# Kernel tuning notes

Hardware: AMD Instinct MI355X
Metric: run time of the kernel (lower is better)

The kernel has to match this reference:

```python
import jax, jax.numpy as jnp
import numpy as np

DILATIONS = (1, 2, 4, 8, 16, 32)
T_ENC = 168   # encoder context length
T_PRED = 24   # predict_sequence_length
FILTERS = 64
FEAT = 15
HIDDEN = 128
B = 2048


def setup_inputs() -> dict:
    key = jax.random.key(0)
    ks = jax.random.split(key, 12)
    w = lambda k, s: jax.random.normal(k, s, jnp.float32) * 0.05
    return {
        "decoder_features": jax.random.normal(ks[0], (B, T_PRED, FEAT), jnp.float32),
        "decoder_init_input": jax.random.normal(ks[1], (B, 1), jnp.float32),
        "encoder_outputs": jax.random.normal(ks[2], (len(DILATIONS), B, T_ENC, FILTERS), jnp.float32),
        "W1": w(ks[3], (FEAT + 1, FILTERS)), "b1": jnp.zeros((FILTERS,), jnp.float32),
        "W2": w(ks[4], (FILTERS, 2 * FILTERS)), "b2": jnp.zeros((2 * FILTERS,), jnp.float32),
        "W3": w(ks[5], (FILTERS, 2 * FILTERS)),
        "W4": w(ks[6], (FILTERS, 2 * FILTERS)), "b4": jnp.zeros((2 * FILTERS,), jnp.float32),
        "W5": w(ks[7], (FILTERS * len(DILATIONS), HIDDEN)), "b5": jnp.zeros((HIDDEN,), jnp.float32),
        "W6": w(ks[8], (HIDDEN, 1)), "b6": jnp.zeros((1,), jnp.float32),
    }


def reference(decoder_features, decoder_init_input, encoder_outputs,
              W1, b1, W2, b2, W3, W4, b4, W5, b5, W6, b6):
    L, Bd, Te, F = encoder_outputs.shape
    # Preallocated growing state buffer (the torch/keras code does tf.concat each step)
    bufs0 = jnp.concatenate(
        [encoder_outputs, jnp.zeros((L, Bd, T_PRED, F), encoder_outputs.dtype)], axis=2)

    def step(bufs, t):
        # Note: the source never updates prev_output, so (eval mode) this_input
        # always uses decoder_init_input concatenated with step-t features.
        this_input = jnp.concatenate(
            [decoder_init_input, decoder_features[:, t]], axis=-1)  # [B, FEAT+1]
        x = jnp.tanh(this_input @ W1 + b1)  # [B, F]
        skips_all = []
        for l, d in enumerate(DILATIONS):
            # encoder_outputs[l][:, -d, :] of a buffer of current length T_ENC + t
            state = jax.lax.dynamic_index_in_dim(
                bufs[l], T_ENC + t - d, axis=1, keepdims=False)  # [B, F]
            dc = state @ W2 + b2 + x @ W3  # [B, 2F]
            f, g = jnp.split(dc, 2, axis=1)
            gated = jnp.tanh(f) * jax.nn.sigmoid(g)  # [B, F]
            out = gated @ W4 + b4  # [B, 2F]
            skips, res = jnp.split(out, 2, axis=1)
            x = x + res
            bufs = bufs.at[l, :, T_ENC + t, :].set(x)
            skips_all.append(skips)
        sk = jax.nn.relu(jnp.concatenate(skips_all, axis=1))  # [B, F*L]
        h = jax.nn.relu(sk @ W5 + b5)  # [B, HIDDEN]
        y = h @ W6 + b6  # [B, 1]
        return bufs, y

    _, ys = jax.lax.scan(step, bufs0, jnp.arange(T_PRED))
    return jnp.transpose(ys, (1, 0, 2))  # [B, T_PRED, 1]
```

## Files before the change

kernel.cpp:

```cpp
#include <hip/hip_runtime.h>
#include <hip/hip_bf16.h>
#include <cstddef>

#define NB 2048
#define TENC 168
#define TPRED 24

typedef _Float16 h8 __attribute__((ext_vector_type(8)));
typedef float f4v __attribute__((ext_vector_type(4)));

#define LBAR() asm volatile("s_waitcnt lgkmcnt(0)\ns_barrier" ::: "memory")

__device__ __forceinline__ float tanh_fast(float v) {
  v = fminf(v, 15.0f);
  const float ex = __expf(2.0f * v);
  return (ex - 1.0f) * __builtin_amdgcn_rcpf(ex + 1.0f);
}
__device__ __forceinline__ float sig_fast(float v) {
  return __builtin_amdgcn_rcpf(1.0f + __expf(-v));
}

#define MFMA16(a, b, c) __builtin_amdgcn_mfma_f32_16x16x32_f16((a), (b), (c), 0, 0, 0)

__global__ __launch_bounds__(512, 1) void dec_phase1(
    const float* __restrict__ feat,
    const float* __restrict__ dinit,
    const float* __restrict__ enc,
    const float* __restrict__ W1,
    const float* __restrict__ b1,
    const float* __restrict__ W2,
    const float* __restrict__ b2,
    const float* __restrict__ W3,
    const float* __restrict__ W4,
    const float* __restrict__ b4,
    _Float16* __restrict__ skbuf,
    int t_steps)
{
  __shared__ _Float16 ring[23][16][72];
  __shared__ _Float16 g16v[2][16][72];
  __shared__ _Float16 xf16[16][72];
  __shared__ float    xf32[64][20];
  __shared__ _Float16 W43h[64][136];

  const int tid = threadIdx.x;
  const int w   = tid >> 6;
  const int ln  = tid & 63;
  const int i   = ln & 15;
  const int q   = ln >> 4;
  const int q8  = q * 8;
  const int e0  = blockIdx.x * 16;

  float* W3s  = (float*)&ring[0][0][0];
  float* W4rs = W3s + 64 * 128;
  for (int idx = tid; idx < 2048; idx += 512)
    ((float4*)W3s)[idx] = ((const float4*)W3)[idx];
  for (int idx = tid; idx < 1024; idx += 512) {
    const int row = idx >> 4, seg = idx & 15;
    *(float4*)&W4rs[row * 64 + seg * 4] = *(const float4*)&W4[row * 128 + 64 + seg * 4];
  }
  __syncthreads();
  {
    const int c = tid & 127, k0 = (tid >> 7) << 4;
    float acc[16];
    #pragma unroll
    for (int r = 0; r < 16; ++r) acc[r] = 0.0f;
    for (int m = 0; m < 64; ++m) {
      const float w3v = W3s[m * 128 + c];
      #pragma unroll
      for (int r = 0; r < 16; ++r) acc[r] += W4rs[(k0 + r) * 64 + m] * w3v;
    }
    #pragma unroll
    for (int r = 0; r < 16; ++r) W43h[k0 + r][c] = (_Float16)acc[r];
  }
  __syncthreads();

  const int fs = w & 3;
  const int cf = 16 * fs + i;
  const int cg = 64 + cf;
  const int cs = 16 * (w - 4) + i;

  h8 BW2f[2], BW2g[2], BW3f[2], BW3g[2], B43f[2], B43g[2], B4s[2], B4r[2];
  float b2f = 0.f, b2g = 0.f, b4s_b = 0.f, b4r_b = 0.f;
  if (w < 4) {
    #pragma unroll
    for (int kk = 0; kk < 2; ++kk)
      #pragma unroll
      for (int j = 0; j < 8; ++j) {
        const int k = kk * 32 + q8 + j;
        BW2f[kk][j] = (_Float16)W2[k * 128 + cf];
        BW2g[kk][j] = (_Float16)W2[k * 128 + cg];
        BW3f[kk][j] = (_Float16)W3[k * 128 + cf];
        BW3g[kk][j] = (_Float16)W3[k * 128 + cg];
        B43f[kk][j] = W43h[k][cf];
        B43g[kk][j] = W43h[k][cg];
      }
    b2f = b2[cf]; b2g = b2[cg];
  } else {
    #pragma unroll
    for (int kk = 0; kk < 2; ++kk)
      #pragma unroll
      for (int j = 0; j < 8; ++j) {
        const int k = kk * 32 + q8 + j;
        B4s[kk][j] = (_Float16)W4[k * 128 + cs];
        B4r[kk][j] = (_Float16)W4[k * 128 + 64 + cs];
      }
    b4s_b = b4[cs]; b4r_b = b4[64 + cs];
  }
  float w1r[16];
  #pragma unroll
  for (int ii = 0; ii < 16; ++ii) w1r[ii] = W1[ii * 64 + ln];
  const float b1r  = b1[ln];
  const float ini0 = dinit[e0 + 2 * w];
  const float ini1 = dinit[e0 + 2 * w + 1];

  for (int idx = tid; idx < 1920; idx += 512) {
    const int c = idx & 7, el = (idx >> 3) & 15, s = idx >> 7;
    int l, j;
    if (s == 0)      { l = 0; j = 0; }
    else if (s < 3)  { l = 1; j = s - 1; }
    else if (s < 7)  { l = 2; j = s - 3; }
    else             { l = 3; j = s - 7; }
    const int d = 1 << l;
    const float* ep = enc + (((size_t)l * NB + e0 + el) * TENC + (TENC + j - d)) * 64 + c * 8;
    h8 hv;
    #pragma unroll
    for (int u = 0; u < 8; ++u) hv[u] = (_Float16)ep[u];
    *(h8*)&ring[s][el][c * 8] = hv;
  }

  #pragma unroll
  for (int s = 0; s < 2; ++s) {
    const int el = 2 * w + s;
    const float* fp = feat + (size_t)(e0 + el) * TPRED * 15;
    float u = b1r + (s ? ini1 : ini0) * w1r[0];
    #pragma unroll
    for (int ii = 0; ii < 15; ++ii) u += fp[ii] * w1r[ii + 1];
    const float xv = tanh_fast(u);
    xf16[el][ln] = (_Float16)xv;
    xf32[ln][el] = xv;
  }
  LBAR();

  f4v Zf = {0,0,0,0}, Zg = {0,0,0,0}, xreg = {0,0,0,0};

  for (int t = 0; t < t_steps; ++t) {
    const int tn = (t + 1 < t_steps) ? t + 1 : t;
    f4v pfa[2], pfb[2], pfc[2];
    float2 pfd[2]; float pfe[2];
    #pragma unroll
    for (int s = 0; s < 2; ++s) {
      const float* fp = feat + ((size_t)(e0 + 2 * w + s) * TPRED + tn) * 15;
      pfa[s] = *(const f4v*)(fp);
      pfb[s] = *(const f4v*)(fp + 4);
      pfc[s] = *(const f4v*)(fp + 8);
      pfd[s] = *(const float2*)(fp + 12);
      pfe[s] = fp[14];
    }

    h8 s0a[4], s1a[4], s4a0, s4a1;
    f4v p4[4], p5[4];
    if (w < 4) {
      const int t4 = (t < 16) ? t : 0;
      const float* e4 = enc + (((size_t)4 * NB + e0 + i) * TENC + (152 + t4)) * 64 + q8;
      const float* e5 = enc + (((size_t)5 * NB + e0 + i) * TENC + (136 + t )) * 64 + q8;
      p4[0] = *(const f4v*)(e4);      p4[1] = *(const f4v*)(e4 + 4);
      p4[2] = *(const f4v*)(e4 + 32); p4[3] = *(const f4v*)(e4 + 36);
      p5[0] = *(const f4v*)(e5);      p5[1] = *(const f4v*)(e5 + 4);
      p5[2] = *(const f4v*)(e5 + 32); p5[3] = *(const f4v*)(e5 + 36);

      #pragma unroll
      for (int l = 0; l < 4; ++l) {
        const int d = 1 << l;
        const int slot = (d - 1) + (t & (d - 1));
        s0a[l] = *(const h8*)&ring[slot][i][q8];
        s1a[l] = *(const h8*)&ring[slot][i][32 + q8];
      }
      {
        const int slot4 = 15 + (t & 7);
        s4a0 = *(const h8*)&ring[slot4][i][q8];
        s4a1 = *(const h8*)&ring[slot4][i][32 + q8];
      }

      const h8 a2 = *(const h8*)&xf16[i][q8];
      const h8 a3 = *(const h8*)&xf16[i][32 + q8];
      Zf = (f4v){0,0,0,0};  Zg = (f4v){0,0,0,0};
      Zf = MFMA16(a2, BW3f[0], Zf); Zf = MFMA16(a3, BW3f[1], Zf);
      Zg = MFMA16(a2, BW3g[0], Zg); Zg = MFMA16(a3, BW3g[1], Zg);

      f4v dcf = Zf, dcg = Zg;
      dcf = MFMA16(s0a[0], BW2f[0], dcf); dcf = MFMA16(s1a[0], BW2f[1], dcf);
      dcg = MFMA16(s0a[0], BW2g[0], dcg); dcg = MFMA16(s1a[0], BW2g[1], dcg);
      #pragma unroll
      for (int r = 0; r < 4; ++r) {
        const float gd = tanh_fast(dcf[r] + b2f) * sig_fast(dcg[r] + b2g);
        g16v[0][4 * q + r][cf] = (_Float16)gd;
      }
    } else {
      xreg = *(const f4v*)&xf32[cs][4 * q];
    }
    LBAR();

    #pragma unroll
    for (int l = 1; l < 6; ++l) {
      const int pm1 = (l - 1) & 1;
      const h8 gA0 = *(const h8*)&g16v[pm1][i][q8];
      const h8 gA1 = *(const h8*)&g16v[pm1][i][32 + q8];

      if (w < 4) {
        Zf = MFMA16(gA0, B43f[0], Zf); Zf = MFMA16(gA1, B43f[1], Zf);
        Zg = MFMA16(gA0, B43g[0], Zg); Zg = MFMA16(gA1, B43g[1], Zg);
        h8 sa0, sa1;
        if (l <= 3) { sa0 = s0a[l]; sa1 = s1a[l]; }
        else if (l == 4) {
          if (t < 16) {
            #pragma unroll
            for (int u = 0; u < 4; ++u) {
              sa0[u] = (_Float16)p4[0][u]; sa0[u + 4] = (_Float16)p4[1][u];
              sa1[u] = (_Float16)p4[2][u]; sa1[u + 4] = (_Float16)p4[3][u];
            }
          } else { sa0 = s4a0; sa1 = s4a1; }
        } else {
          #pragma unroll
          for (int u = 0; u < 4; ++u) {
            sa0[u] = (_Float16)p5[0][u]; sa0[u + 4] = (_Float16)p5[1][u];
            sa1[u] = (_Float16)p5[2][u]; sa1[u + 4] = (_Float16)p5[3][u];
          }
        }
        f4v dcf = Zf, dcg = Zg;
        dcf = MFMA16(sa0, BW2f[0], dcf); dcf = MFMA16(sa1, BW2f[1], dcf);
        dcg = MFMA16(sa0, BW2g[0], dcg); dcg = MFMA16(sa1, BW2g[1], dcg);
        #pragma unroll
        for (int r = 0; r < 4; ++r) {
          const float gd = tanh_fast(dcf[r] + b2f) * sig_fast(dcg[r] + b2g);
          g16v[l & 1][4 * q + r][cf] = (_Float16)gd;
        }
      } else {
        const int lp  = l - 1;
        const int dlp = 1 << lp;
        const int slotlp = (lp <= 3) ? (dlp - 1) + (t & (dlp - 1)) : 15 + (t & 7);
        f4v osk = {0,0,0,0}, ore = {0,0,0,0};
        osk = MFMA16(gA0, B4s[0], osk); osk = MFMA16(gA1, B4s[1], osk);
        ore = MFMA16(gA0, B4r[0], ore); ore = MFMA16(gA1, B4r[1], ore);
        const bool wr = (t + dlp) <= 23;
        #pragma unroll
        for (int r = 0; r < 4; ++r) {
          skbuf[((size_t)(e0 + 4 * q + r) * TPRED + t) * 384 + lp * 64 + cs] =
              (_Float16)fmaxf(osk[r] + b4s_b, 0.0f);
          const float xn = xreg[r] + ore[r] + b4r_b;
          xreg[r] = xn;
          if (wr) ring[slotlp][4 * q + r][cs] = (_Float16)xn;
        }
      }
      LBAR();
    }

    if (w >= 4) {
      const h8 gA0 = *(const h8*)&g16v[1][i][q8];
      const h8 gA1 = *(const h8*)&g16v[1][i][32 + q8];
      f4v osk = {0,0,0,0};
      osk = MFMA16(gA0, B4s[0], osk); osk = MFMA16(gA1, B4s[1], osk);
      #pragma unroll
      for (int r = 0; r < 4; ++r)
        skbuf[((size_t)(e0 + 4 * q + r) * TPRED + t) * 384 + 5 * 64 + cs] =
            (_Float16)fmaxf(osk[r] + b4s_b, 0.0f);
    }
    if (t + 1 < t_steps) {
      #pragma unroll
      for (int s = 0; s < 2; ++s) {
        const int el = 2 * w + s;
        float u = b1r + (s ? ini1 : ini0) * w1r[0];
        u += pfa[s][0] * w1r[1]  + pfa[s][1] * w1r[2]  + pfa[s][2] * w1r[3]  + pfa[s][3] * w1r[4];
        u += pfb[s][0] * w1r[5]  + pfb[s][1] * w1r[6]  + pfb[s][2] * w1r[7]  + pfb[s][3] * w1r[8];
        u += pfc[s][0] * w1r[9]  + pfc[s][1] * w1r[10] + pfc[s][2] * w1r[11] + pfc[s][3] * w1r[12];
        u += pfd[s].x  * w1r[13] + pfd[s].y  * w1r[14] + pfe[s]    * w1r[15];
        const float xv = tanh_fast(u);
        xf16[el][ln] = (_Float16)xv;
        xf32[ln][el] = xv;
      }
    }
    LBAR();
  }
}

__global__ __launch_bounds__(512, 1) void dec_phase2(
    const _Float16* __restrict__ skbuf,
    const float* __restrict__ W5,
    const float* __restrict__ b5,
    const float* __restrict__ W6,
    const float* __restrict__ b6,
    float* __restrict__ out)
{
  __shared__ _Float16 As[192][392];
  __shared__ float red[192][8];

  const int tid = threadIdx.x;
  const int w   = tid >> 6;
  const int ln  = tid & 63;
  const int i   = ln & 15;
  const int q   = ln >> 4;
  const int R0  = blockIdx.x * 192;
  const int col = 16 * w + i;

  h8 B5[12];
  #pragma unroll
  for (int kk = 0; kk < 12; ++kk)
    #pragma unroll
    for (int j = 0; j < 8; ++j)
      B5[kk][j] = (_Float16)W5[(size_t)(kk * 32 + q * 8 + j) * 128 + col];
  const float b5r = b5[col], w6r = W6[col];

  h8 v1[9], v2[9];
  #pragma unroll
  for (int it = 0; it < 9; ++it) {
    const int idx = tid + it * 512;
    v1[it] = *(const h8*)&skbuf[(size_t)(R0 + idx / 48) * 384 + (idx % 48) * 8];
  }
  #pragma unroll
  for (int it = 0; it < 9; ++it) {
    const int idx = 4608 + tid + it * 512;
    v2[it] = *(const h8*)&skbuf[(size_t)(R0 + idx / 48) * 384 + (idx % 48) * 8];
  }
  #pragma unroll
  for (int it = 0; it < 9; ++it) {
    const int idx = tid + it * 512;
    *(h8*)&As[idx / 48][(idx % 48) * 8] = v1[it];
  }
  __syncthreads();
  #pragma unroll
  for (int it = 0; it < 9; ++it) {
    const int idx = 4608 + tid + it * 512;
    *(h8*)&As[idx / 48][(idx % 48) * 8] = v2[it];
  }

  #pragma unroll
  for (int m = 0; m < 12; ++m) {
    if (m == 6) __syncthreads();
    f4v acc = {0,0,0,0};
    #pragma unroll
    for (int kk = 0; kk < 12; ++kk) {
      const h8 a = *(const h8*)&As[16 * m + i][kk * 32 + q * 8];
      acc = MFMA16(a, B5[kk], acc);
    }
    float py[4];
    #pragma unroll
    for (int r = 0; r < 4; ++r)
      py[r] = fmaxf(acc[r] + b5r, 0.0f) * w6r;
    #pragma unroll
    for (int r = 0; r < 4; ++r) {
      float v = py[r];
      v += __shfl_xor(v, 1);
      v += __shfl_xor(v, 2);
      v += __shfl_xor(v, 4);
      v += __shfl_xor(v, 8);
      py[r] = v;
    }
    if (i == 0) {
      #pragma unroll
      for (int r = 0; r < 4; ++r) red[16 * m + 4 * q + r][w] = py[r];
    }
  }
  __syncthreads();

  if (tid < 192) {
    const f4v r0 = *(const f4v*)&red[tid][0];
    const f4v r1 = *(const f4v*)&red[tid][4];
    out[R0 + tid] = b6[0] + r0[0] + r0[1] + r0[2] + r0[3]
                          + r1[0] + r1[1] + r1[2] + r1[3];
  }
}

extern "C" void kernel_launch(void* const* d_in, const int* in_sizes, int n_in,
                              void* d_out, int out_size, void* d_ws, size_t ws_size,
                              hipStream_t stream) {
  const float* feat  = (const float*)d_in[0];
  const float* dinit = (const float*)d_in[1];
  const float* enc   = (const float*)d_in[2];
  const float* W1    = (const float*)d_in[3];
  const float* b1    = (const float*)d_in[4];
  const float* W2    = (const float*)d_in[5];
  const float* b2    = (const float*)d_in[6];
  const float* W3    = (const float*)d_in[7];
  const float* W4    = (const float*)d_in[8];
  const float* b4    = (const float*)d_in[9];
  const float* W5    = (const float*)d_in[10];
  const float* b5    = (const float*)d_in[11];
  const float* W6    = (const float*)d_in[12];
  const float* b6    = (const float*)d_in[13];

  float*     out   = (float*)d_out;
  _Float16*  skbuf = (_Float16*)d_ws;

  dec_phase1<<<dim3(128), dim3(512), 0, stream>>>(
      feat, dinit, enc, W1, b1, W2, b2, W3, W4, b4, skbuf, TPRED);
  dec_phase2<<<dim3(256), dim3(512), 0, stream>>>(
      skbuf, W5, b5, W6, b6, out);
}
```

Before: 117.7 us.

## Split decoder into flag-synchronized producer/consumer warp groups and halve phase2 tiles

Phase1 now splits its work into two warp groups with roles. Warps 0-3 run the serial gate chain (the W3 and W43 contributions plus the gating). Warps 4-7 precompute the state@W2 terms for all six layers, the next step's input projection, and the skip/residual outputs, and the two groups talk through LDS flag polling instead of block-wide barriers. This lets the off-critical-path work overlap with the dependent gate chain, at the cost of spin-wait polling, which has a guard that breaks out after a fixed count. Phase2 uses 96-row tiles across 512 blocks instead of 192-row tiles across 256, and the double-buffered load staging is removed.

```diff
diff --git a/kernel.cpp b/kernel.cpp
--- a/kernel.cpp
+++ b/kernel.cpp
@@ -9,18 +9,33 @@
 typedef _Float16 h8 __attribute__((ext_vector_type(8)));
 typedef float f4v __attribute__((ext_vector_type(4)));
 
-#define LBAR() asm volatile("s_waitcnt lgkmcnt(0)\ns_barrier" ::: "memory")
-
-__device__ __forceinline__ float tanh_fast(float v) {
-  v = fminf(v, 15.0f);
-  const float ex = __expf(2.0f * v);
-  return (ex - 1.0f) * __builtin_amdgcn_rcpf(ex + 1.0f);
-}
-__device__ __forceinline__ float sig_fast(float v) {
-  return __builtin_amdgcn_rcpf(1.0f + __expf(-v));
-}
-
 #define MFMA16(a, b, c) __builtin_amdgcn_mfma_f32_16x16x32_f16((a), (b), (c), 0, 0, 0)
+
+__device__ __forceinline__ float gate_fast(float a, float g) {
+  a = fminf(a, 15.0f);
+  const float e2a = __builtin_amdgcn_exp2f(a * 2.88539008177793f);
+  const float eg  = __builtin_amdgcn_exp2f(g * -1.44269504088896f);
+  return (e2a - 1.0f) * __builtin_amdgcn_rcpf((e2a + 1.0f) * (1.0f + eg));
+}
+__device__ __forceinline__ float tanh_fast(float u) {
+  const float e2 = __builtin_amdgcn_exp2f(fminf(u, 15.0f) * 2.88539008177793f);
+  return (e2 - 1.0f) * __builtin_amdgcn_rcpf(e2 + 1.0f);
+}
+
+__device__ __forceinline__ void poll4(volatile int* f, int tgt) {
+  int guard = 0;
+  while (f[0] < tgt || f[1] < tgt || f[2] < tgt || f[3] < tgt) {
+    __builtin_amdgcn_s_sleep(1);
+    if (++guard > 200000) break;
+  }
+  asm volatile("" ::: "memory");
+}
+
+#define FLAG_SET(slotp, v)                                  \
+  do {                                                      \
+    asm volatile("s_waitcnt lgkmcnt(0)" ::: "memory");      \
+    if (ln == 0) *(volatile int*)(slotp) = (v);             \
+  } while (0)
 
 __global__ __launch_bounds__(512, 1) void dec_phase1(
     const float* __restrict__ feat,
@@ -37,10 +52,11 @@
     int t_steps)
 {
   __shared__ _Float16 ring[23][16][72];
-  __shared__ _Float16 g16v[2][16][72];
-  __shared__ _Float16 xf16[16][72];
-  __shared__ float    xf32[64][20];
-  __shared__ _Float16 W43h[64][136];
+  __shared__ _Float16 g16v[2][6][16][72];
+  __shared__ _Float16 xf16[2][16][72];
+  __shared__ float    xf32[2][64][20];
+  __shared__ float    S32[6][2][64][20];
+  __shared__ int      flags[16];
 
   const int tid = threadIdx.x;
   const int w   = tid >> 6;
@@ -59,6 +75,8 @@
     *(float4*)&W4rs[row * 64 + seg * 4] = *(const float4*)&W4[row * 128 + 64 + seg * 4];
   }
   __syncthreads();
+
+  _Float16* W43h = (_Float16*)&S32[0][0][0][0];
   {
     const int c = tid & 127, k0 = (tid >> 7) << 4;
     float acc[16];
@@ -70,48 +88,44 @@
       for (int r = 0; r < 16; ++r) acc[r] += W4rs[(k0 + r) * 64 + m] * w3v;
     }
     #pragma unroll
-    for (int r = 0; r < 16; ++r) W43h[k0 + r][c] = (_Float16)acc[r];
+    for (int r = 0; r < 16; ++r) W43h[(k0 + r) * 136 + c] = (_Float16)acc[r];
   }
   __syncthreads();
 
-  const int fs = w & 3;
-  const int cf = 16 * fs + i;
+  h8 BA[2], BB[2], BC[2], BD[2];
+  float c2f = 0.f, c2g = 0.f, c4s = 0.f, c4r = 0.f;
+  float w1r[16]; float b1r = 0.f; float ini4[4] = {0.f, 0.f, 0.f, 0.f};
+  const int cf = (w < 4) ? (16 * w + i) : (16 * (w - 4) + i);
   const int cg = 64 + cf;
-  const int cs = 16 * (w - 4) + i;
-
-  h8 BW2f[2], BW2g[2], BW3f[2], BW3g[2], B43f[2], B43g[2], B4s[2], B4r[2];
-  float b2f = 0.f, b2g = 0.f, b4s_b = 0.f, b4r_b = 0.f;
   if (w < 4) {
     #pragma unroll
     for (int kk = 0; kk < 2; ++kk)
       #pragma unroll
       for (int j = 0; j < 8; ++j) {
         const int k = kk * 32 + q8 + j;
-        BW2f[kk][j] = (_Float16)W2[k * 128 + cf];
-        BW2g[kk][j] = (_Float16)W2[k * 128 + cg];
-        BW3f[kk][j] = (_Float16)W3[k * 128 + cf];
-        BW3g[kk][j] = (_Float16)W3[k * 128 + cg];
-        B43f[kk][j] = W43h[k][cf];
-        B43g[kk][j] = W43h[k][cg];
-      }
-    b2f = b2[cf]; b2g = b2[cg];
+        BA[kk][j] = (_Float16)W3[k * 128 + cf];
+        BB[kk][j] = (_Float16)W3[k * 128 + cg];
+        BC[kk][j] = W43h[k * 136 + cf];
+        BD[kk][j] = W43h[k * 136 + cg];
+      }
   } else {
     #pragma unroll
     for (int kk = 0; kk < 2; ++kk)
       #pragma unroll
       for (int j = 0; j < 8; ++j) {
         const int k = kk * 32 + q8 + j;
-        B4s[kk][j] = (_Float16)W4[k * 128 + cs];
-        B4r[kk][j] = (_Float16)W4[k * 128 + 64 + cs];
-      }
-    b4s_b = b4[cs]; b4r_b = b4[64 + cs];
-  }
-  float w1r[16];
-  #pragma unroll
-  for (int ii = 0; ii < 16; ++ii) w1r[ii] = W1[ii * 64 + ln];
-  const float b1r  = b1[ln];
-  const float ini0 = dinit[e0 + 2 * w];
-  const float ini1 = dinit[e0 + 2 * w + 1];
+        BA[kk][j] = (_Float16)W2[k * 128 + cf];
+        BB[kk][j] = (_Float16)W2[k * 128 + cg];
+        BC[kk][j] = (_Float16)W4[k * 128 + cf];
+        BD[kk][j] = (_Float16)W4[k * 128 + cg];
+      }
+    c2f = b2[cf]; c2g = b2[cg]; c4s = b4[cf]; c4r = b4[cg];
+    #pragma unroll
+    for (int ii = 0; ii < 16; ++ii) w1r[ii] = W1[ii * 64 + ln];
+    b1r = b1[ln];
+    #pragma unroll
+    for (int s = 0; s < 4; ++s) ini4[s] = dinit[e0 + 4 * (w - 4) + s];
+  }
 
   for (int idx = tid; idx < 1920; idx += 512) {
     const int c = idx & 7, el = (idx >> 3) & 15, s = idx >> 7;
@@ -127,98 +141,97 @@
     for (int u = 0; u < 8; ++u) hv[u] = (_Float16)ep[u];
     *(h8*)&ring[s][el][c * 8] = hv;
   }
-
-  #pragma unroll
-  for (int s = 0; s < 2; ++s) {
-    const int el = 2 * w + s;
-    const float* fp = feat + (size_t)(e0 + el) * TPRED * 15;
-    float u = b1r + (s ? ini1 : ini0) * w1r[0];
-    #pragma unroll
-    for (int ii = 0; ii < 15; ++ii) u += fp[ii] * w1r[ii + 1];
-    const float xv = tanh_fast(u);
-    xf16[el][ln] = (_Float16)xv;
-    xf32[ln][el] = xv;
-  }
-  LBAR();
-
-  f4v Zf = {0,0,0,0}, Zg = {0,0,0,0}, xreg = {0,0,0,0};
-
-  for (int t = 0; t < t_steps; ++t) {
-    const int tn = (t + 1 < t_steps) ? t + 1 : t;
-    f4v pfa[2], pfb[2], pfc[2];
-    float2 pfd[2]; float pfe[2];
+  {
+    float w1e[16];
+    #pragma unroll
+    for (int ii = 0; ii < 16; ++ii) w1e[ii] = W1[ii * 64 + ln];
+    const float b1e = b1[ln];
     #pragma unroll
     for (int s = 0; s < 2; ++s) {
-      const float* fp = feat + ((size_t)(e0 + 2 * w + s) * TPRED + tn) * 15;
-      pfa[s] = *(const f4v*)(fp);
-      pfb[s] = *(const f4v*)(fp + 4);
-      pfc[s] = *(const f4v*)(fp + 8);
-      pfd[s] = *(const float2*)(fp + 12);
-      pfe[s] = fp[14];
-    }
-
-    h8 s0a[4], s1a[4], s4a0, s4a1;
+      const int el = 2 * w + s;
+      const float* fp = feat + (size_t)(e0 + el) * TPRED * 15;
+      float u = b1e + dinit[e0 + el] * w1e[0];
+      #pragma unroll
+      for (int ii = 0; ii < 15; ++ii) u += fp[ii] * w1e[ii + 1];
+      const float xv = tanh_fast(u);
+      xf16[0][el][ln] = (_Float16)xv;
+      xf32[0][ln][el] = xv;
+    }
+  }
+  if (tid < 16) flags[tid] = (tid >= 8 && tid < 12) ? 1 : 0;
+  __syncthreads();
+
+  if (w < 4) {
+    for (int t = 0; t < t_steps; ++t) {
+      poll4(&flags[8],  t + 1);
+      poll4(&flags[4],  t + 1);
+      poll4(&flags[12], t);
+
+      f4v Sf[6], Sg[6];
+      #pragma unroll
+      for (int l = 0; l < 6; ++l) {
+        Sf[l] = *(const f4v*)&S32[l][0][cf][4 * q];
+        Sg[l] = *(const f4v*)&S32[l][1][cf][4 * q];
+      }
+      const h8 a2 = *(const h8*)&xf16[t & 1][i][q8];
+      const h8 a3 = *(const h8*)&xf16[t & 1][i][32 + q8];
+      f4v Zf = {0, 0, 0, 0}, Zg = {0, 0, 0, 0};
+      Zf = MFMA16(a2, BA[0], Zf); Zf = MFMA16(a3, BA[1], Zf);
+      Zg = MFMA16(a2, BB[0], Zg); Zg = MFMA16(a3, BB[1], Zg);
+      #pragma unroll
+      for (int r = 0; r < 4; ++r)
+        g16v[t & 1][0][4 * q + r][cf] =
+            (_Float16)gate_fast(Zf[r] + Sf[0][r], Zg[r] + Sg[0][r]);
+      FLAG_SET(&flags[w], 6 * t + 1);
+
+      #pragma unroll
+      for (int l = 1; l < 6; ++l) {
+        poll4(&flags[0], 6 * t + l);
+        const h8 gA0 = *(const h8*)&g16v[t & 1][l - 1][i][q8];
+        const h8 gA1 = *(const h8*)&g16v[t & 1][l - 1][i][32 + q8];
+        Zf = MFMA16(gA0, BC[0], Zf); Zf = MFMA16(gA1, BC[1], Zf);
+        Zg = MFMA16(gA0, BD[0], Zg); Zg = MFMA16(gA1, BD[1], Zg);
+        #pragma unroll
+        for (int r = 0; r < 4; ++r)
+          g16v[t & 1][l][4 * q + r][cf] =
+              (_Float16)gate_fast(Zf[r] + Sf[l][r], Zg[r] + Sg[l][r]);
+        FLAG_SET(&flags[w], 6 * t + l + 1);
+      }
+    }
+  } else {
+    const int cw = w - 4;
     f4v p4[4], p5[4];
-    if (w < 4) {
-      const int t4 = (t < 16) ? t : 0;
-      const float* e4 = enc + (((size_t)4 * NB + e0 + i) * TENC + (152 + t4)) * 64 + q8;
-      const float* e5 = enc + (((size_t)5 * NB + e0 + i) * TENC + (136 + t )) * 64 + q8;
+    {
+      const float* e4 = enc + (((size_t)4 * NB + e0 + i) * TENC + 152) * 64 + q8;
+      const float* e5 = enc + (((size_t)5 * NB + e0 + i) * TENC + 136) * 64 + q8;
       p4[0] = *(const f4v*)(e4);      p4[1] = *(const f4v*)(e4 + 4);
       p4[2] = *(const f4v*)(e4 + 32); p4[3] = *(const f4v*)(e4 + 36);
       p5[0] = *(const f4v*)(e5);      p5[1] = *(const f4v*)(e5 + 4);
       p5[2] = *(const f4v*)(e5 + 32); p5[3] = *(const f4v*)(e5 + 36);
-
-      #pragma unroll
-      for (int l = 0; l < 4; ++l) {
-        const int d = 1 << l;
-        const int slot = (d - 1) + (t & (d - 1));
-        s0a[l] = *(const h8*)&ring[slot][i][q8];
-        s1a[l] = *(const h8*)&ring[slot][i][32 + q8];
-      }
-      {
-        const int slot4 = 15 + (t & 7);
-        s4a0 = *(const h8*)&ring[slot4][i][q8];
-        s4a1 = *(const h8*)&ring[slot4][i][32 + q8];
-      }
-
-      const h8 a2 = *(const h8*)&xf16[i][q8];
-      const h8 a3 = *(const h8*)&xf16[i][32 + q8];
-      Zf = (f4v){0,0,0,0};  Zg = (f4v){0,0,0,0};
-      Zf = MFMA16(a2, BW3f[0], Zf); Zf = MFMA16(a3, BW3f[1], Zf);
-      Zg = MFMA16(a2, BW3g[0], Zg); Zg = MFMA16(a3, BW3g[1], Zg);
-
-      f4v dcf = Zf, dcg = Zg;
-      dcf = MFMA16(s0a[0], BW2f[0], dcf); dcf = MFMA16(s1a[0], BW2f[1], dcf);
-      dcg = MFMA16(s0a[0], BW2g[0], dcg); dcg = MFMA16(s1a[0], BW2g[1], dcg);
-      #pragma unroll
-      for (int r = 0; r < 4; ++r) {
-        const float gd = tanh_fast(dcf[r] + b2f) * sig_fast(dcg[r] + b2g);
-        g16v[0][4 * q + r][cf] = (_Float16)gd;
-      }
-    } else {
-      xreg = *(const f4v*)&xf32[cs][4 * q];
-    }
-    LBAR();
-
-    #pragma unroll
-    for (int l = 1; l < 6; ++l) {
-      const int pm1 = (l - 1) & 1;
-      const h8 gA0 = *(const h8*)&g16v[pm1][i][q8];
-      const h8 gA1 = *(const h8*)&g16v[pm1][i][32 + q8];
-
-      if (w < 4) {
-        Zf = MFMA16(gA0, B43f[0], Zf); Zf = MFMA16(gA1, B43f[1], Zf);
-        Zg = MFMA16(gA0, B43g[0], Zg); Zg = MFMA16(gA1, B43g[1], Zg);
+    }
+    f4v xregA = {0, 0, 0, 0}, xregB = {0, 0, 0, 0};
+
+    for (int t = 0; t < t_steps; ++t) {
+      poll4(&flags[12], t);
+      #pragma unroll
+      for (int l = 0; l < 6; ++l) {
         h8 sa0, sa1;
-        if (l <= 3) { sa0 = s0a[l]; sa1 = s1a[l]; }
-        else if (l == 4) {
+        if (l <= 3) {
+          const int d = 1 << l, slot = (d - 1) + (t & (d - 1));
+          sa0 = *(const h8*)&ring[slot][i][q8];
+          sa1 = *(const h8*)&ring[slot][i][32 + q8];
+        } else if (l == 4) {
           if (t < 16) {
             #pragma unroll
             for (int u = 0; u < 4; ++u) {
               sa0[u] = (_Float16)p4[0][u]; sa0[u + 4] = (_Float16)p4[1][u];
               sa1[u] = (_Float16)p4[2][u]; sa1[u + 4] = (_Float16)p4[3][u];
             }
-          } else { sa0 = s4a0; sa1 = s4a1; }
+          } else {
+            const int slot = 15 + (t & 7);
+            sa0 = *(const h8*)&ring[slot][i][q8];
+            sa1 = *(const h8*)&ring[slot][i][32 + q8];
+          }
         } else {
           #pragma unroll
           for (int u = 0; u < 4; ++u) {
@@ -226,59 +239,102 @@
             sa1[u] = (_Float16)p5[2][u]; sa1[u + 4] = (_Float16)p5[3][u];
           }
         }
-        f4v dcf = Zf, dcg = Zg;
-        dcf = MFMA16(sa0, BW2f[0], dcf); dcf = MFMA16(sa1, BW2f[1], dcf);
-        dcg = MFMA16(sa0, BW2g[0], dcg); dcg = MFMA16(sa1, BW2g[1], dcg);
+        f4v Sfa = {c2f, c2f, c2f, c2f}, Sga = {c2g, c2g, c2g, c2g};
+        Sfa = MFMA16(sa0, BA[0], Sfa); Sfa = MFMA16(sa1, BA[1], Sfa);
+        Sga = MFMA16(sa0, BB[0], Sga); Sga = MFMA16(sa1, BB[1], Sga);
+        *(f4v*)&S32[l][0][cf][4 * q] = Sfa;
+        *(f4v*)&S32[l][1][cf][4 * q] = Sga;
+      }
+      FLAG_SET(&flags[4 + cw], t + 1);
+
+      if (t + 1 < t_steps) {
+        if (t + 1 < 16) {
+          const float* e4 = enc + (((size_t)4 * NB + e0 + i) * TENC + (152 + t + 1)) * 64 + q8;
+          p4[0] = *(const f4v*)(e4);      p4[1] = *(const f4v*)(e4 + 4);
+          p4[2] = *(const f4v*)(e4 + 32); p4[3] = *(const f4v*)(e4 + 36);
+        }
+        const float* e5 = enc + (((size_t)5 * NB + e0 + i) * TENC + (136 + t + 1)) * 64 + q8;
+        p5[0] = *(const f4v*)(e5);      p5[1] = *(const f4v*)(e5 + 4);
+        p5[2] = *(const f4v*)(e5 + 32); p5[3] = *(const f4v*)(e5 + 36);
+
+        #pragma unroll
+        for (int s = 0; s < 4; ++s) {
+          const int el = 4 * cw + s;
+          const float* fp = feat + ((size_t)(e0 + el) * TPRED + (t + 1)) * 15;
+          float u = b1r + ini4[s] * w1r[0];
+          #pragma unroll
+          for (int ii = 0; ii < 15; ++ii) u += fp[ii] * w1r[ii + 1];
+          const float xv = tanh_fast(u);
+          xf16[(t + 1) & 1][el][ln] = (_Float16)xv;
+          xf32[(t + 1) & 1][ln][el] = xv;
+        }
+        FLAG_SET(&flags[8 + cw], t + 2);
+      }
+
+      if (t > 0) {
+        const int s = t - 1;
+        poll4(&flags[0], 6 * s + 6);
+        #pragma unroll
+        for (int lp = 1; lp < 6; ++lp) {
+          const h8 gA0 = *(const h8*)&g16v[s & 1][lp][i][q8];
+          const h8 gA1 = *(const h8*)&g16v[s & 1][lp][i][32 + q8];
+          f4v osk = {c4s, c4s, c4s, c4s};
+          osk = MFMA16(gA0, BC[0], osk); osk = MFMA16(gA1, BC[1], osk);
+          #pragma unroll
+          for (int r = 0; r < 4; ++r)
+            skbuf[((size_t)(e0 + 4 * q + r) * TPRED + s) * 384 + lp * 64 + cf] =
+                (_Float16)fmaxf(osk[r], 0.0f);
+          if (lp < 5) {
+            f4v ore = {c4r, c4r, c4r, c4r};
+            ore = MFMA16(gA0, BD[0], ore); ore = MFMA16(gA1, BD[1], ore);
+            const int dlp = 1 << lp;
+            const int slot = (lp <= 3) ? (dlp - 1) + (s & (dlp - 1)) : 15 + (s & 7);
+            const bool wr = (lp <= 3) || (s <= 7);
+            #pragma unroll
+            for (int r = 0; r < 4; ++r) {
+              xregA[r] += ore[r];
+              if (wr) ring[slot][4 * q + r][cf] = (_Float16)xregA[r];
+            }
+          }
+        }
+      }
+
+      poll4(&flags[4], t + 1);
+      poll4(&flags[0], 6 * t + 1);
+      {
+        const h8 gA0 = *(const h8*)&g16v[t & 1][0][i][q8];
+        const h8 gA1 = *(const h8*)&g16v[t & 1][0][i][32 + q8];
+        f4v osk = {c4s, c4s, c4s, c4s}, ore = {c4r, c4r, c4r, c4r};
+        osk = MFMA16(gA0, BC[0], osk); osk = MFMA16(gA1, BC[1], osk);
+        ore = MFMA16(gA0, BD[0], ore); ore = MFMA16(gA1, BD[1], ore);
+        xregB = *(const f4v*)&xf32[t & 1][cf][4 * q];
         #pragma unroll
         for (int r = 0; r < 4; ++r) {
-          const float gd = tanh_fast(dcf[r] + b2f) * sig_fast(dcg[r] + b2g);
-          g16v[l & 1][4 * q + r][cf] = (_Float16)gd;
+          skbuf[((size_t)(e0 + 4 * q + r) * TPRED + t) * 384 + cf] =
+              (_Float16)fmaxf(osk[r], 0.0f);
+          xregB[r] += ore[r];
+          ring[0][4 * q + r][cf] = (_Float16)xregB[r];
         }
-      } else {
-        const int lp  = l - 1;
-        const int dlp = 1 << lp;
-        const int slotlp = (lp <= 3) ? (dlp - 1) + (t & (dlp - 1)) : 15 + (t & 7);
-        f4v osk = {0,0,0,0}, ore = {0,0,0,0};
-        osk = MFMA16(gA0, B4s[0], osk); osk = MFMA16(gA1, B4s[1], osk);
-        ore = MFMA16(gA0, B4r[0], ore); ore = MFMA16(gA1, B4r[1], ore);
-        const bool wr = (t + dlp) <= 23;
+      }
+      FLAG_SET(&flags[12 + cw], t + 1);
+      xregA = xregB;
+    }
+
+    {
+      const int s = t_steps - 1;
+      poll4(&flags[0], 6 * s + 6);
+      #pragma unroll
+      for (int lp = 1; lp < 6; ++lp) {
+        const h8 gA0 = *(const h8*)&g16v[s & 1][lp][i][q8];
+        const h8 gA1 = *(const h8*)&g16v[s & 1][lp][i][32 + q8];
+        f4v osk = {c4s, c4s, c4s, c4s};
+        osk = MFMA16(gA0, BC[0], osk); osk = MFMA16(gA1, BC[1], osk);
         #pragma unroll
-        for (int r = 0; r < 4; ++r) {
-          skbuf[((size_t)(e0 + 4 * q + r) * TPRED + t) * 384 + lp * 64 + cs] =
-              (_Float16)fmaxf(osk[r] + b4s_b, 0.0f);
-          const float xn = xreg[r] + ore[r] + b4r_b;
-          xreg[r] = xn;
-          if (wr) ring[slotlp][4 * q + r][cs] = (_Float16)xn;
-        }
-      }
-      LBAR();
-    }
-
-    if (w >= 4) {
-      const h8 gA0 = *(const h8*)&g16v[1][i][q8];
-      const h8 gA1 = *(const h8*)&g16v[1][i][32 + q8];
-      f4v osk = {0,0,0,0};
-      osk = MFMA16(gA0, B4s[0], osk); osk = MFMA16(gA1, B4s[1], osk);
-      #pragma unroll
-      for (int r = 0; r < 4; ++r)
-        skbuf[((size_t)(e0 + 4 * q + r) * TPRED + t) * 384 + 5 * 64 + cs] =
-            (_Float16)fmaxf(osk[r] + b4s_b, 0.0f);
-    }
-    if (t + 1 < t_steps) {
-      #pragma unroll
-      for (int s = 0; s < 2; ++s) {
-        const int el = 2 * w + s;
-        float u = b1r + (s ? ini1 : ini0) * w1r[0];
-        u += pfa[s][0] * w1r[1]  + pfa[s][1] * w1r[2]  + pfa[s][2] * w1r[3]  + pfa[s][3] * w1r[4];
-        u += pfb[s][0] * w1r[5]  + pfb[s][1] * w1r[6]  + pfb[s][2] * w1r[7]  + pfb[s][3] * w1r[8];
-        u += pfc[s][0] * w1r[9]  + pfc[s][1] * w1r[10] + pfc[s][2] * w1r[11] + pfc[s][3] * w1r[12];
-        u += pfd[s].x  * w1r[13] + pfd[s].y  * w1r[14] + pfe[s]    * w1r[15];
-        const float xv = tanh_fast(u);
-        xf16[el][ln] = (_Float16)xv;
-        xf32[ln][el] = xv;
-      }
-    }
-    LBAR();
+        for (int r = 0; r < 4; ++r)
+          skbuf[((size_t)(e0 + 4 * q + r) * TPRED + s) * 384 + lp * 64 + cf] =
+              (_Float16)fmaxf(osk[r], 0.0f);
+      }
+    }
   }
 }
 
@@ -290,15 +346,15 @@
     const float* __restrict__ b6,
     float* __restrict__ out)
 {
-  __shared__ _Float16 As[192][392];
-  __shared__ float red[192][8];
+  __shared__ _Float16 As[96][392];
+  __shared__ float red[96][8];
 
   const int tid = threadIdx.x;
   const int w   = tid >> 6;
   const int ln  = tid & 63;
   const int i   = ln & 15;
   const int q   = ln >> 4;
-  const int R0  = blockIdx.x * 192;
+  const int R0  = blockIdx.x * 96;
   const int col = 16 * w + i;
 
   h8 B5[12];
@@ -309,33 +365,17 @@
       B5[kk][j] = (_Float16)W5[(size_t)(kk * 32 + q * 8 + j) * 128 + col];
   const float b5r = b5[col], w6r = W6[col];
 
-  h8 v1[9], v2[9];
   #pragma unroll
   for (int it = 0; it < 9; ++it) {
     const int idx = tid + it * 512;
-    v1[it] = *(const h8*)&skbuf[(size_t)(R0 + idx / 48) * 384 + (idx % 48) * 8];
-  }
+    const h8 v = *(const h8*)&skbuf[(size_t)(R0 + idx / 48) * 384 + (idx % 48) * 8];
+    *(h8*)&As[idx / 48][(idx % 48) * 8] = v;
+  }
+  __syncthreads();
+
   #pragma unroll
-  for (int it = 0; it < 9; ++it) {
-    const int idx = 4608 + tid + it * 512;
-    v2[it] = *(const h8*)&skbuf[(size_t)(R0 + idx / 48) * 384 + (idx % 48) * 8];
-  }
-  #pragma unroll
-  for (int it = 0; it < 9; ++it) {
-    const int idx = tid + it * 512;
-    *(h8*)&As[idx / 48][(idx % 48) * 8] = v1[it];
-  }
-  __syncthreads();
-  #pragma unroll
-  for (int it = 0; it < 9; ++it) {
-    const int idx = 4608 + tid + it * 512;
-    *(h8*)&As[idx / 48][(idx % 48) * 8] = v2[it];
-  }
-
-  #pragma unroll
-  for (int m = 0; m < 12; ++m) {
-    if (m == 6) __syncthreads();
-    f4v acc = {0,0,0,0};
+  for (int m = 0; m < 6; ++m) {
+    f4v acc = {0, 0, 0, 0};
     #pragma unroll
     for (int kk = 0; kk < 12; ++kk) {
       const h8 a = *(const h8*)&As[16 * m + i][kk * 32 + q * 8];
@@ -361,7 +401,7 @@
   }
   __syncthreads();
 
-  if (tid < 192) {
+  if (tid < 96) {
     const f4v r0 = *(const f4v*)&red[tid][0];
     const f4v r1 = *(const f4v*)&red[tid][4];
     out[R0 + tid] = b6[0] + r0[0] + r0[1] + r0[2] + r0[3]
@@ -392,6 +432,6 @@
 
   dec_phase1<<<dim3(128), dim3(512), 0, stream>>>(
       feat, dinit, enc, W1, b1, W2, b2, W3, W4, b4, skbuf, TPRED);
-  dec_phase2<<<dim3(256), dim3(512), 0, stream>>>(
+  dec_phase2<<<dim3(512), dim3(512), 0, stream>>>(
       skbuf, W5, b5, W6, b6, out);
 }
```

New measurement: 148.1 us. 25.9% more time.
